# Kernel tuning notes

Hardware: AMD Instinct MI355X
Metric: run time of the kernel (lower is better)

## Reference

```python
import jax, jax.numpy as jnp
import numpy as np

NUM_BOND_TYPE = 6
NUM_BOND_DIRECTION = 3
N_NODES = 20000
N_EDGES = 320000
HIDDEN = 256
OUT = 256
N_MASK = 2000


def setup_inputs() -> dict:
    key = jax.random.key(0)
    ks = jax.random.split(key, 12)
    x = jax.random.normal(ks[0], (N_NODES, HIDDEN), dtype=jnp.float32)
    edge_index = jax.random.randint(ks[1], (2, N_EDGES), 0, N_NODES, dtype=jnp.int64)
    edge_attr = jax.random.randint(ks[2], (N_EDGES, 2), 0, 3, dtype=jnp.int64)
    mask_node_indices = jax.random.randint(ks[3], (N_MASK,), 0, N_NODES, dtype=jnp.int64)
    # parameters (torch Linear convention: y = x @ W.T + b)
    def xavier(k, shape):
        fan_in, fan_out = shape[1], shape[0]
        lim = float(np.sqrt(6.0 / (fan_in + fan_out)))
        return jax.random.uniform(k, shape, jnp.float32, -lim, lim)
    prelu_a = jnp.asarray(0.25, dtype=jnp.float32)  # torch PReLU default
    W_enc = xavier(ks[4], (HIDDEN, HIDDEN))          # enc_to_dec, no bias
    E1 = xavier(ks[5], (NUM_BOND_TYPE, HIDDEN))
    E2 = xavier(ks[6], (NUM_BOND_DIRECTION, HIDDEN))
    W1 = xavier(ks[7], (2 * HIDDEN, HIDDEN))
    b1 = jnp.zeros((2 * HIDDEN,), jnp.float32)
    W2 = xavier(ks[8], (OUT, 2 * HIDDEN))
    b2 = jnp.zeros((OUT,), jnp.float32)
    return {"x": x, "edge_index": edge_index, "edge_attr": edge_attr,
            "mask_node_indices": mask_node_indices, "prelu_a": prelu_a,
            "W_enc": W_enc, "E1": E1, "E2": E2,
            "W1": W1, "b1": b1, "W2": W2, "b2": b2}


def reference(x, edge_index, edge_attr, mask_node_indices, prelu_a,
              W_enc, E1, E2, W1, b1, W2, b2):
    N = x.shape[0]
    # PReLU -> enc_to_dec linear (no bias) -> zero masked rows
    x = jnp.where(x >= 0, x, prelu_a * x)
    x = x @ W_enc.T
    x = x.at[mask_node_indices].set(0.0)
    # add self loops: (i,i) edges with attr (4, 0)
    loop = jnp.arange(N, dtype=edge_index.dtype)
    ei = jnp.concatenate([edge_index, jnp.stack([loop, loop])], axis=1)  # [2, E+N]
    loop_attr = jnp.concatenate(
        [jnp.full((N, 1), 4, edge_attr.dtype), jnp.zeros((N, 1), edge_attr.dtype)], axis=1)
    ea = jnp.concatenate([edge_attr, loop_attr], axis=0)                 # [E+N, 2]
    edge_emb = E1[ea[:, 0]] + E2[ea[:, 1]]                               # [E+N, D]
    src, dst = ei[0], ei[1]                                              # j -> i
    msg = x[src] + edge_emb                                              # [E+N, D]
    aggr = jax.ops.segment_sum(msg, dst, num_segments=N)                 # [N, D]
    # GIN MLP: Linear -> ReLU -> Linear
    h = jax.nn.relu(aggr @ W1.T + b1)
    return h @ W2.T + b2
```

## Files before the change

### kernel.cpp

```cpp
#include <hip/hip_runtime.h>

#define HIDDEN 256
#define CAP 64

typedef _Float16 h4_t __attribute__((ext_vector_type(4)));
typedef _Float16 h8_t __attribute__((ext_vector_type(8)));
typedef float    f4_t __attribute__((ext_vector_type(4)));

typedef const __attribute__((address_space(1))) void* gbl_ptr_t;
typedef __attribute__((address_space(3))) void*       lds_ptr_t;

__device__ inline f4_t cvt4(h4_t h) {
    f4_t o; o.x = (float)h.x; o.y = (float)h.y; o.z = (float)h.z; o.w = (float)h.w;
    return o;
}

__global__ __launch_bounds__(256) void k_prep(
        const float* __restrict__ x, _Float16* __restrict__ xh,
        const float* __restrict__ prelu_a, int M, int Mpad, int nb_x,
        const int* __restrict__ ei, const int* __restrict__ ea, int E,
        int* __restrict__ cnt, int* __restrict__ csr, int nb_fill,
        const float* __restrict__ W_enc, const float* __restrict__ W1,
        const float* __restrict__ W2, _Float16* __restrict__ Whenc,
        _Float16* __restrict__ Wh1, _Float16* __restrict__ Wh2, int nb_w,
        const int* __restrict__ mask, unsigned char* __restrict__ flags, int NM) {
    int b = blockIdx.x;
    int t = threadIdx.x;
    if (b < nb_x) {
        int base = (b * 256 + t) * 4;
        if (base >= Mpad * HIDDEN) return;
        int row = base >> 8;
        h4_t o;
        if (row < M) {
            float pa = *prelu_a;
            f4_t v = *(const f4_t*)(x + base);
            o.x = (_Float16)(v.x >= 0.f ? v.x : pa * v.x);
            o.y = (_Float16)(v.y >= 0.f ? v.y : pa * v.y);
            o.z = (_Float16)(v.z >= 0.f ? v.z : pa * v.z);
            o.w = (_Float16)(v.w >= 0.f ? v.w : pa * v.w);
        } else {
            o = (h4_t)(_Float16)0.f;
        }
        *(h4_t*)(xh + base) = o;
        return;
    }
    b -= nb_x;
    if (b < nb_fill) {
        int e = b * 256 + t;
        if (e >= E) return;
        int src = ei[e];
        int dst = ei[E + e];
        int combo = ea[2 * e] * 3 + ea[2 * e + 1];
        int slot = atomicAdd(&cnt[dst], 1);
        if (slot < CAP) csr[dst * CAP + slot] = src | (combo << 16);
        return;
    }
    b -= nb_fill;
    if (b < nb_w) {
        const int n0 = HIDDEN * HIDDEN, n1 = 2 * HIDDEN * HIDDEN, n2 = HIDDEN * 2 * HIDDEN;
        int base = (b * 256 + t) * 4;
        const float* s; _Float16* d; int off;
        if (base < n0) { s = W_enc; d = Whenc; off = base; }
        else if (base < n0 + n1) { s = W1; d = Wh1; off = base - n0; }
        else if (base < n0 + n1 + n2) { s = W2; d = Wh2; off = base - n0 - n1; }
        else return;
        f4_t v = *(const f4_t*)(s + off);
        h4_t o; o.x = (_Float16)v.x; o.y = (_Float16)v.y;
        o.z = (_Float16)v.z; o.w = (_Float16)v.w;
        *(h4_t*)(d + off) = o;
        return;
    }
    b -= nb_w;
    {
        int i = b * 256 + t;
        if (i < NM) flags[mask[i]] = 1;
    }
}

__global__ __launch_bounds__(256) void k_aggregate(
        const _Float16* __restrict__ xe,
        const float* __restrict__ E1, const float* __restrict__ E2,
        const int* __restrict__ cnt, const int* __restrict__ csr,
        _Float16* __restrict__ aggr, int N, int Mpad) {
    __shared__ __align__(16) _Float16 e12h[18 * HIDDEN];
    int t = threadIdx.x;
    for (int idx = t; idx < 18 * 64; idx += 256) {
        int combo = idx >> 6, c4 = (idx & 63) * 4;
        int a1 = combo / 3, a2 = combo - a1 * 3;
        f4_t v1 = *(const f4_t*)(E1 + a1 * HIDDEN + c4);
        f4_t v2 = *(const f4_t*)(E2 + a2 * HIDDEN + c4);
        h4_t o;
        o.x = (_Float16)(v1.x + v2.x); o.y = (_Float16)(v1.y + v2.y);
        o.z = (_Float16)(v1.z + v2.z); o.w = (_Float16)(v1.w + v2.w);
        *(h4_t*)(e12h + combo * HIDDEN + c4) = o;
    }
    __syncthreads();
    int node = blockIdx.x * 4 + (t >> 6);
    if (node >= Mpad) return;
    int lane = t & 63;
    int c0 = lane * 4;
    if (node >= N) {
        *(h4_t*)(aggr + (size_t)node * HIDDEN + c0) = (h4_t)(_Float16)0.f;
        return;
    }
    int deg = cnt[node];
    if (deg > CAP) deg = CAP;
    const int* lst = csr + (size_t)node * CAP;
    int pv = (lane < deg) ? lst[lane] : 0;

    h4_t hs = *(const h4_t*)(xe + (size_t)node * HIDDEN + c0);
    h4_t se = *(const h4_t*)(e12h + 12 * HIDDEN + c0);
    f4_t acc = cvt4(hs) + cvt4(se);

    int e = 0;
    for (; e + 7 < deg; e += 8) {
        int p[8]; h4_t hv[8], qv[8];
#pragma unroll
        for (int j = 0; j < 8; ++j) p[j] = __shfl(pv, e + j, 64);
#pragma unroll
        for (int j = 0; j < 8; ++j)
            hv[j] = *(const h4_t*)(xe + (size_t)(p[j] & 0xFFFF) * HIDDEN + c0);
#pragma unroll
        for (int j = 0; j < 8; ++j)
            qv[j] = *(const h4_t*)(e12h + (p[j] >> 16) * HIDDEN + c0);
        h4_t s0 = (hv[0] + qv[0]) + (hv[1] + qv[1]);
        h4_t s1 = (hv[2] + qv[2]) + (hv[3] + qv[3]);
        h4_t s2 = (hv[4] + qv[4]) + (hv[5] + qv[5]);
        h4_t s3 = (hv[6] + qv[6]) + (hv[7] + qv[7]);
        acc += cvt4(s0) + cvt4(s1);
        acc += cvt4(s2) + cvt4(s3);
    }
    for (; e < deg; ++e) {
        int p = __shfl(pv, e, 64);
        h4_t h = *(const h4_t*)(xe + (size_t)(p & 0xFFFF) * HIDDEN + c0);
        h4_t q = *(const h4_t*)(e12h + (p >> 16) * HIDDEN + c0);
        acc += cvt4(h + q);
    }
    h4_t o;
    o.x = (_Float16)acc.x; o.y = (_Float16)acc.y;
    o.z = (_Float16)acc.z; o.w = (_Float16)acc.w;
    *(h4_t*)(aggr + (size_t)node * HIDDEN + c0) = o;
}

template <int TM, int K, bool RELU, bool HAS_BIAS, bool OUT_F16, bool MASK>
__global__ __launch_bounds__(64) void k_gemm64(
        const _Float16* __restrict__ A, const _Float16* __restrict__ B,
        const float* __restrict__ bias, void* __restrict__ Cout,
        const unsigned char* __restrict__ flags, int Mstore, int N) {
    constexpr int BM = TM * 16;
    __shared__ __align__(16) _Float16 As[BM * 32];
    __shared__ __align__(16) _Float16 Bs[64 * 32];
    int L = threadIdx.x;
    int m0 = blockIdx.x * BM, n0 = blockIdx.y * 64;
    int lr = L & 15, lk = (L >> 4) * 8;

    f4_t acc[TM][4] = {};

    auto stage = [&](int k0) {
#pragma unroll
        for (int i = 0; i < TM; ++i) {
            int c = L + 64 * i;
            __builtin_amdgcn_global_load_lds(
                (gbl_ptr_t)(A + (size_t)(m0 + (c >> 2)) * K + k0 + (c & 3) * 8),
                (lds_ptr_t)(As + c * 8), 16, 0, 0);
        }
#pragma unroll
        for (int i = 0; i < 4; ++i) {
            int c = L + 64 * i;
            __builtin_amdgcn_global_load_lds(
                (gbl_ptr_t)(B + (size_t)(n0 + (c >> 2)) * K + k0 + (c & 3) * 8),
                (lds_ptr_t)(Bs + c * 8), 16, 0, 0);
        }
    };

    stage(0);
    constexpr int NS = K / 32;
#pragma unroll
    for (int s = 0; s < NS; ++s) {
        asm volatile("s_waitcnt vmcnt(0)" ::: "memory");
        h8_t af[TM], bf[4];
#pragma unroll
        for (int i = 0; i < TM; ++i) af[i] = *(const h8_t*)&As[(i * 16 + lr) * 32 + lk];
#pragma unroll
        for (int j = 0; j < 4; ++j)  bf[j] = *(const h8_t*)&Bs[(j * 16 + lr) * 32 + lk];
        asm volatile("s_waitcnt lgkmcnt(0)" ::: "memory");
        if (s + 1 < NS) stage((s + 1) * 32);
#pragma unroll
        for (int i = 0; i < TM; ++i)
#pragma unroll
            for (int j = 0; j < 4; ++j)
                acc[i][j] = __builtin_amdgcn_mfma_f32_16x16x32_f16(af[i], bf[j], acc[i][j], 0, 0, 0);
    }

    int lr4 = (L >> 4) * 4;
#pragma unroll
    for (int i = 0; i < TM; ++i)
#pragma unroll
        for (int r = 0; r < 4; ++r) {
            int row = m0 + i * 16 + lr4 + r;
            float zm = (MASK && flags[row]) ? 0.f : 1.f;
#pragma unroll
            for (int j = 0; j < 4; ++j) {
                int col = n0 + j * 16 + lr;
                float v = acc[i][j][r];
                if (HAS_BIAS) v += bias[col];
                if (RELU) v = v > 0.f ? v : 0.f;
                v *= zm;
                if (OUT_F16) {
                    ((_Float16*)Cout)[(size_t)row * N + col] = (_Float16)v;
                } else {
                    if (row < Mstore) ((float*)Cout)[(size_t)row * N + col] = v;
                }
            }
        }
}

__global__ __launch_bounds__(256) void k_mlp(
        const _Float16* __restrict__ AG, const _Float16* __restrict__ W1h,
        const float* __restrict__ b1, const _Float16* __restrict__ W2h,
        const float* __restrict__ b2, float* __restrict__ out, int Mstore) {
    __shared__ __align__(16) _Float16 Hs[16][32 * 32];
    __shared__ __align__(16) _Float16 st[4][3072];
    int t = threadIdx.x;
    int w = t >> 6, L = t & 63;
    int lr = L & 15, lk = (L >> 4) * 8, lr4 = (L >> 4) * 4;
    int m0 = blockIdx.x * 32;
    _Float16* As = st[w];
    _Float16* Bs = st[w] + 1024;

#pragma unroll
    for (int p = 0; p < 2; ++p) {
        int nb0 = 64 * (w + 4 * p);
        auto stage1 = [&](int k0) {
#pragma unroll
            for (int i = 0; i < 2; ++i) {
                int c = L + 64 * i;
                __builtin_amdgcn_global_load_lds(
                    (gbl_ptr_t)(AG + (size_t)(m0 + (c >> 2)) * 256 + k0 + (c & 3) * 8),
                    (lds_ptr_t)(As + c * 8), 16, 0, 0);
            }
#pragma unroll
            for (int i = 0; i < 4; ++i) {
                int c = L + 64 * i;
                __builtin_amdgcn_global_load_lds(
                    (gbl_ptr_t)(W1h + (size_t)(nb0 + (c >> 2)) * 256 + k0 + (c & 3) * 8),
                    (lds_ptr_t)(Bs + c * 8), 16, 0, 0);
            }
        };
        f4_t acc[2][4] = {};
        stage1(0);
#pragma unroll
        for (int s = 0; s < 8; ++s) {
            asm volatile("s_waitcnt vmcnt(0)" ::: "memory");
            h8_t af[2], bf[4];
#pragma unroll
            for (int i = 0; i < 2; ++i) af[i] = *(const h8_t*)&As[(i * 16 + lr) * 32 + lk];
#pragma unroll
            for (int j = 0; j < 4; ++j) bf[j] = *(const h8_t*)&Bs[(j * 16 + lr) * 32 + lk];
            asm volatile("s_waitcnt lgkmcnt(0)" ::: "memory");
            if (s + 1 < 8) stage1((s + 1) * 32);
#pragma unroll
            for (int i = 0; i < 2; ++i)
#pragma unroll
                for (int j = 0; j < 4; ++j)
                    acc[i][j] = __builtin_amdgcn_mfma_f32_16x16x32_f16(af[i], bf[j], acc[i][j], 0, 0, 0);
        }
        float b1v[4];
#pragma unroll
        for (int j = 0; j < 4; ++j) b1v[j] = b1[nb0 + j * 16 + lr];
#pragma unroll
        for (int i = 0; i < 2; ++i)
#pragma unroll
            for (int r = 0; r < 4; ++r) {
                int row = i * 16 + lr4 + r;
#pragma unroll
                for (int j = 0; j < 4; ++j) {
                    int col = nb0 + j * 16 + lr;
                    float v = acc[i][j][r] + b1v[j];
                    v = v > 0.f ? v : 0.f;
                    Hs[col >> 5][row * 32 + (col & 31)] = (_Float16)v;
                }
            }
    }
    __syncthreads();

    int n0 = w * 64;
    auto stage2 = [&](int k0) {
#pragma unroll
        for (int i = 0; i < 4; ++i) {
            int c = L + 64 * i;
            __builtin_amdgcn_global_load_lds(
                (gbl_ptr_t)(W2h + (size_t)(n0 + (c >> 2)) * 512 + k0 + (c & 3) * 8),
                (lds_ptr_t)(Bs + c * 8), 16, 0, 0);
        }
    };
    f4_t acc[2][4] = {};
    stage2(0);
#pragma unroll
    for (int s = 0; s < 16; ++s) {
        asm volatile("s_waitcnt vmcnt(0)" ::: "memory");
        h8_t af[2], bf[4];
#pragma unroll
        for (int i = 0; i < 2; ++i) af[i] = *(const h8_t*)&Hs[s][(i * 16 + lr) * 32 + lk];
#pragma unroll
        for (int j = 0; j < 4; ++j) bf[j] = *(const h8_t*)&Bs[(j * 16 + lr) * 32 + lk];
        asm volatile("s_waitcnt lgkmcnt(0)" ::: "memory");
        if (s + 1 < 16) stage2((s + 1) * 32);
#pragma unroll
        for (int i = 0; i < 2; ++i)
#pragma unroll
            for (int j = 0; j < 4; ++j)
                acc[i][j] = __builtin_amdgcn_mfma_f32_16x16x32_f16(af[i], bf[j], acc[i][j], 0, 0, 0);
    }
    float b2v[4];
#pragma unroll
    for (int j = 0; j < 4; ++j) b2v[j] = b2[n0 + j * 16 + lr];
#pragma unroll
    for (int i = 0; i < 2; ++i)
#pragma unroll
        for (int r = 0; r < 4; ++r) {
            int row = m0 + i * 16 + lr4 + r;
            if (row < Mstore) {
#pragma unroll
                for (int j = 0; j < 4; ++j) {
                    int col = n0 + j * 16 + lr;
                    out[(size_t)row * 256 + col] = acc[i][j][r] + b2v[j];
                }
            }
        }
}

extern "C" void kernel_launch(void* const* d_in, const int* in_sizes, int n_in,
                              void* d_out, int out_size, void* d_ws, size_t ws_size,
                              hipStream_t stream) {
    const float* x       = (const float*)d_in[0];
    const int*   ei      = (const int*)d_in[1];
    const int*   ea      = (const int*)d_in[2];
    const int*   mask    = (const int*)d_in[3];
    const float* prelu_a = (const float*)d_in[4];
    const float* W_enc   = (const float*)d_in[5];
    const float* E1      = (const float*)d_in[6];
    const float* E2      = (const float*)d_in[7];
    const float* W1      = (const float*)d_in[8];
    const float* b1      = (const float*)d_in[9];
    const float* W2      = (const float*)d_in[10];
    const float* b2      = (const float*)d_in[11];
    float*       out     = (float*)d_out;

    int N  = in_sizes[0] / HIDDEN;
    int E  = in_sizes[1] / 2;
    int NM = in_sizes[3];
    int Mpad = ((N + 127) / 128) * 128;

    char* ws = (char*)d_ws;
    size_t off = 0;
    _Float16* xh    = (_Float16*)(ws + off); off += (size_t)Mpad * HIDDEN * 2;
    _Float16* XEh   = (_Float16*)(ws + off); off += (size_t)Mpad * HIDDEN * 2;
    _Float16* AGh   = (_Float16*)(ws + off); off += (size_t)Mpad * HIDDEN * 2;
    _Float16* Whenc = (_Float16*)(ws + off); off += (size_t)HIDDEN * HIDDEN * 2;
    _Float16* Wh1   = (_Float16*)(ws + off); off += (size_t)2 * HIDDEN * HIDDEN * 2;
    _Float16* Wh2   = (_Float16*)(ws + off); off += (size_t)HIDDEN * 2 * HIDDEN * 2;
    int* cnt        = (int*)(ws + off);      off += (size_t)N * 4;
    unsigned char* flags = (unsigned char*)(ws + off); off += (size_t)Mpad;
    off = (off + 15) & ~(size_t)15;
    int* csr        = (int*)(ws + off);      off += (size_t)N * CAP * 4;

    hipMemsetAsync(cnt, 0, (size_t)N * 4 + (size_t)Mpad, stream);

    int nb_x    = (Mpad * HIDDEN / 4 + 255) / 256;
    int nb_fill = (E + 255) / 256;
    int wtot4   = (HIDDEN * HIDDEN + 2 * HIDDEN * HIDDEN + HIDDEN * 2 * HIDDEN) / 4;
    int nb_w    = (wtot4 + 255) / 256;
    int nb_m    = (NM + 255) / 256;
    k_prep<<<nb_x + nb_fill + nb_w + nb_m, 256, 0, stream>>>(
        x, xh, prelu_a, N, Mpad, nb_x,
        ei, ea, E, cnt, csr, nb_fill,
        W_enc, W1, W2, Whenc, Wh1, Wh2, nb_w,
        mask, flags, NM);

    dim3 g1(Mpad / 32, HIDDEN / 64);
    k_gemm64<2, HIDDEN, false, false, true, true><<<g1, 64, 0, stream>>>(
        xh, Whenc, nullptr, XEh, flags, N, HIDDEN);

    k_aggregate<<<(Mpad + 3) / 4, 256, 0, stream>>>(XEh, E1, E2, cnt, csr, AGh, N, Mpad);

    k_mlp<<<Mpad / 32, 256, 0, stream>>>(AGh, Wh1, b1, Wh2, b2, out, N);
}
```

Baseline: 186.3 us.

## Multi-buffer GEMM loads and split fused MLP into two pipelined GEMMs

The generic MFMA GEMM now keeps four LDS stages in flight, using compile-time unrolled steps with partial vmcnt waits instead of a full wait every k-step. Its tile grows from 32 to 64 rows. The fused two-layer MLP kernel is removed and replaced by two launches of this GEMM, with the hidden activation written to an fp16 global buffer. This trades extra global traffic for the intermediate and one more launch against better load/compute overlap and more compute per block.

```diff
diff --git a/kernel.cpp b/kernel.cpp
--- a/kernel.cpp
+++ b/kernel.cpp
@@ -9,6 +9,17 @@
 
 typedef const __attribute__((address_space(1))) void* gbl_ptr_t;
 typedef __attribute__((address_space(3))) void*       lds_ptr_t;
+
+template<int N> struct IC { static constexpr int v = N; };
+template<int...> struct Seq {};
+template<int N, int... Is> struct MkSeq : MkSeq<N - 1, N - 1, Is...> {};
+template<int... Is> struct MkSeq<0, Is...> { using t = Seq<Is...>; };
+template<typename F, int... Is>
+__device__ __forceinline__ void unroll_for(F&& f, Seq<Is...>) { (f(IC<Is>{}), ...); }
+
+template<int N> __device__ __forceinline__ void vmwait() {
+    asm volatile("s_waitcnt vmcnt(%0)" :: "n"(N) : "memory");
+}
 
 __device__ inline f4_t cvt4(h4_t h) {
     f4_t o; o.x = (float)h.x; o.y = (float)h.y; o.z = (float)h.z; o.w = (float)h.w;
@@ -147,50 +158,57 @@
         const _Float16* __restrict__ A, const _Float16* __restrict__ B,
         const float* __restrict__ bias, void* __restrict__ Cout,
         const unsigned char* __restrict__ flags, int Mstore, int N) {
-    constexpr int BM = TM * 16;
-    __shared__ __align__(16) _Float16 As[BM * 32];
-    __shared__ __align__(16) _Float16 Bs[64 * 32];
+    constexpr int BM  = TM * 16;
+    constexpr int RB  = 4;
+    constexpr int NS  = K / 32;
+    constexpr int LPS = TM + 4;
+    __shared__ __align__(16) _Float16 As[RB][BM * 32];
+    __shared__ __align__(16) _Float16 Bs[RB][64 * 32];
     int L = threadIdx.x;
     int m0 = blockIdx.x * BM, n0 = blockIdx.y * 64;
     int lr = L & 15, lk = (L >> 4) * 8;
 
     f4_t acc[TM][4] = {};
 
-    auto stage = [&](int k0) {
+    auto stage = [&](int s) {
+        int k0 = s * 32, r = s & (RB - 1);
 #pragma unroll
         for (int i = 0; i < TM; ++i) {
             int c = L + 64 * i;
             __builtin_amdgcn_global_load_lds(
                 (gbl_ptr_t)(A + (size_t)(m0 + (c >> 2)) * K + k0 + (c & 3) * 8),
-                (lds_ptr_t)(As + c * 8), 16, 0, 0);
+                (lds_ptr_t)(As[r] + c * 8), 16, 0, 0);
         }
 #pragma unroll
         for (int i = 0; i < 4; ++i) {
             int c = L + 64 * i;
             __builtin_amdgcn_global_load_lds(
                 (gbl_ptr_t)(B + (size_t)(n0 + (c >> 2)) * K + k0 + (c & 3) * 8),
-                (lds_ptr_t)(Bs + c * 8), 16, 0, 0);
+                (lds_ptr_t)(Bs[r] + c * 8), 16, 0, 0);
         }
     };
 
-    stage(0);
-    constexpr int NS = K / 32;
-#pragma unroll
-    for (int s = 0; s < NS; ++s) {
-        asm volatile("s_waitcnt vmcnt(0)" ::: "memory");
+    unroll_for([&](auto P) { stage(P.v); }, typename MkSeq<RB>::t{});
+
+    unroll_for([&](auto SC) {
+        constexpr int s = SC.v;
+        constexpr int issued = (RB + s < NS) ? RB + s : NS;
+        vmwait<(issued - s - 1) * LPS>();
         h8_t af[TM], bf[4];
-#pragma unroll
-        for (int i = 0; i < TM; ++i) af[i] = *(const h8_t*)&As[(i * 16 + lr) * 32 + lk];
-#pragma unroll
-        for (int j = 0; j < 4; ++j)  bf[j] = *(const h8_t*)&Bs[(j * 16 + lr) * 32 + lk];
+        const _Float16* as = As[s & (RB - 1)];
+        const _Float16* bs = Bs[s & (RB - 1)];
+#pragma unroll
+        for (int i = 0; i < TM; ++i) af[i] = *(const h8_t*)&as[(i * 16 + lr) * 32 + lk];
+#pragma unroll
+        for (int j = 0; j < 4; ++j)  bf[j] = *(const h8_t*)&bs[(j * 16 + lr) * 32 + lk];
         asm volatile("s_waitcnt lgkmcnt(0)" ::: "memory");
-        if (s + 1 < NS) stage((s + 1) * 32);
+        if constexpr (s + RB < NS) stage(s + RB);
 #pragma unroll
         for (int i = 0; i < TM; ++i)
 #pragma unroll
             for (int j = 0; j < 4; ++j)
                 acc[i][j] = __builtin_amdgcn_mfma_f32_16x16x32_f16(af[i], bf[j], acc[i][j], 0, 0, 0);
-    }
+    }, typename MkSeq<NS>::t{});
 
     int lr4 = (L >> 4) * 4;
 #pragma unroll
@@ -210,121 +228,6 @@
                     ((_Float16*)Cout)[(size_t)row * N + col] = (_Float16)v;
                 } else {
                     if (row < Mstore) ((float*)Cout)[(size_t)row * N + col] = v;
-                }
-            }
-        }
-}
-
-__global__ __launch_bounds__(256) void k_mlp(
-        const _Float16* __restrict__ AG, const _Float16* __restrict__ W1h,
-        const float* __restrict__ b1, const _Float16* __restrict__ W2h,
-        const float* __restrict__ b2, float* __restrict__ out, int Mstore) {
-    __shared__ __align__(16) _Float16 Hs[16][32 * 32];
-    __shared__ __align__(16) _Float16 st[4][3072];
-    int t = threadIdx.x;
-    int w = t >> 6, L = t & 63;
-    int lr = L & 15, lk = (L >> 4) * 8, lr4 = (L >> 4) * 4;
-    int m0 = blockIdx.x * 32;
-    _Float16* As = st[w];
-    _Float16* Bs = st[w] + 1024;
-
-#pragma unroll
-    for (int p = 0; p < 2; ++p) {
-        int nb0 = 64 * (w + 4 * p);
-        auto stage1 = [&](int k0) {
-#pragma unroll
-            for (int i = 0; i < 2; ++i) {
-                int c = L + 64 * i;
-                __builtin_amdgcn_global_load_lds(
-                    (gbl_ptr_t)(AG + (size_t)(m0 + (c >> 2)) * 256 + k0 + (c & 3) * 8),
-                    (lds_ptr_t)(As + c * 8), 16, 0, 0);
-            }
-#pragma unroll
-            for (int i = 0; i < 4; ++i) {
-                int c = L + 64 * i;
-                __builtin_amdgcn_global_load_lds(
-                    (gbl_ptr_t)(W1h + (size_t)(nb0 + (c >> 2)) * 256 + k0 + (c & 3) * 8),
-                    (lds_ptr_t)(Bs + c * 8), 16, 0, 0);
-            }
-        };
-        f4_t acc[2][4] = {};
-        stage1(0);
-#pragma unroll
-        for (int s = 0; s < 8; ++s) {
-            asm volatile("s_waitcnt vmcnt(0)" ::: "memory");
-            h8_t af[2], bf[4];
-#pragma unroll
-            for (int i = 0; i < 2; ++i) af[i] = *(const h8_t*)&As[(i * 16 + lr) * 32 + lk];
-#pragma unroll
-            for (int j = 0; j < 4; ++j) bf[j] = *(const h8_t*)&Bs[(j * 16 + lr) * 32 + lk];
-            asm volatile("s_waitcnt lgkmcnt(0)" ::: "memory");
-            if (s + 1 < 8) stage1((s + 1) * 32);
-#pragma unroll
-            for (int i = 0; i < 2; ++i)
-#pragma unroll
-                for (int j = 0; j < 4; ++j)
-                    acc[i][j] = __builtin_amdgcn_mfma_f32_16x16x32_f16(af[i], bf[j], acc[i][j], 0, 0, 0);
-        }
-        float b1v[4];
-#pragma unroll
-        for (int j = 0; j < 4; ++j) b1v[j] = b1[nb0 + j * 16 + lr];
-#pragma unroll
-        for (int i = 0; i < 2; ++i)
-#pragma unroll
-            for (int r = 0; r < 4; ++r) {
-                int row = i * 16 + lr4 + r;
-#pragma unroll
-                for (int j = 0; j < 4; ++j) {
-                    int col = nb0 + j * 16 + lr;
-                    float v = acc[i][j][r] + b1v[j];
-                    v = v > 0.f ? v : 0.f;
-                    Hs[col >> 5][row * 32 + (col & 31)] = (_Float16)v;
-                }
-            }
-    }
-    __syncthreads();
-
-    int n0 = w * 64;
-    auto stage2 = [&](int k0) {
-#pragma unroll
-        for (int i = 0; i < 4; ++i) {
-            int c = L + 64 * i;
-            __builtin_amdgcn_global_load_lds(
-                (gbl_ptr_t)(W2h + (size_t)(n0 + (c >> 2)) * 512 + k0 + (c & 3) * 8),
-                (lds_ptr_t)(Bs + c * 8), 16, 0, 0);
-        }
-    };
-    f4_t acc[2][4] = {};
-    stage2(0);
-#pragma unroll
-    for (int s = 0; s < 16; ++s) {
-        asm volatile("s_waitcnt vmcnt(0)" ::: "memory");
-        h8_t af[2], bf[4];
-#pragma unroll
-        for (int i = 0; i < 2; ++i) af[i] = *(const h8_t*)&Hs[s][(i * 16 + lr) * 32 + lk];
-#pragma unroll
-        for (int j = 0; j < 4; ++j) bf[j] = *(const h8_t*)&Bs[(j * 16 + lr) * 32 + lk];
-        asm volatile("s_waitcnt lgkmcnt(0)" ::: "memory");
-        if (s + 1 < 16) stage2((s + 1) * 32);
-#pragma unroll
-        for (int i = 0; i < 2; ++i)
-#pragma unroll
-            for (int j = 0; j < 4; ++j)
-                acc[i][j] = __builtin_amdgcn_mfma_f32_16x16x32_f16(af[i], bf[j], acc[i][j], 0, 0, 0);
-    }
-    float b2v[4];
-#pragma unroll
-    for (int j = 0; j < 4; ++j) b2v[j] = b2[n0 + j * 16 + lr];
-#pragma unroll
-    for (int i = 0; i < 2; ++i)
-#pragma unroll
-        for (int r = 0; r < 4; ++r) {
-            int row = m0 + i * 16 + lr4 + r;
-            if (row < Mstore) {
-#pragma unroll
-                for (int j = 0; j < 4; ++j) {
-                    int col = n0 + j * 16 + lr;
-                    out[(size_t)row * 256 + col] = acc[i][j][r] + b2v[j];
                 }
             }
         }
@@ -357,6 +260,7 @@
     _Float16* xh    = (_Float16*)(ws + off); off += (size_t)Mpad * HIDDEN * 2;
     _Float16* XEh   = (_Float16*)(ws + off); off += (size_t)Mpad * HIDDEN * 2;
     _Float16* AGh   = (_Float16*)(ws + off); off += (size_t)Mpad * HIDDEN * 2;
+    _Float16* Hh    = (_Float16*)(ws + off); off += (size_t)Mpad * 2 * HIDDEN * 2;
     _Float16* Whenc = (_Float16*)(ws + off); off += (size_t)HIDDEN * HIDDEN * 2;
     _Float16* Wh1   = (_Float16*)(ws + off); off += (size_t)2 * HIDDEN * HIDDEN * 2;
     _Float16* Wh2   = (_Float16*)(ws + off); off += (size_t)HIDDEN * 2 * HIDDEN * 2;
@@ -378,11 +282,17 @@
         W_enc, W1, W2, Whenc, Wh1, Wh2, nb_w,
         mask, flags, NM);
 
-    dim3 g1(Mpad / 32, HIDDEN / 64);
-    k_gemm64<2, HIDDEN, false, false, true, true><<<g1, 64, 0, stream>>>(
+    dim3 g1(Mpad / 64, HIDDEN / 64);
+    k_gemm64<4, HIDDEN, false, false, true, true><<<g1, 64, 0, stream>>>(
         xh, Whenc, nullptr, XEh, flags, N, HIDDEN);
 
     k_aggregate<<<(Mpad + 3) / 4, 256, 0, stream>>>(XEh, E1, E2, cnt, csr, AGh, N, Mpad);
 
-    k_mlp<<<Mpad / 32, 256, 0, stream>>>(AGh, Wh1, b1, Wh2, b2, out, N);
-}
+    dim3 g2(Mpad / 64, 2 * HIDDEN / 64);
+    k_gemm64<4, HIDDEN, true, true, true, false><<<g2, 64, 0, stream>>>(
+        AGh, Wh1, b1, Hh, nullptr, N, 2 * HIDDEN);
+
+    dim3 g3(Mpad / 64, HIDDEN / 64);
+    k_gemm64<4, 2 * HIDDEN, false, true, false, false><<<g3, 64, 0, stream>>>(
+        Hh, Wh2, b2, out, nullptr, N, HIDDEN);
+}
```

Result: slower. 207.6 us (+11.5%).
